# Kernel tuning notes

Measured on AMD Instinct MI355X. Metric: run time of the kernel, lower is better.

## Reference

```python
import jax, jax.numpy as jnp
import numpy as np

D_MODEL = 768
NUM_HEADS = 8
HEAD_DIM = D_MODEL // NUM_HEADS


def setup_inputs() -> dict:
    key = jax.random.key(0)
    ks = jax.random.split(key, 5)
    B, N = 4, 2048
    scale = 1.0 / np.sqrt(D_MODEL)
    return {
        "x": jax.random.normal(ks[0], (B, N, D_MODEL), dtype=jnp.float32),
        "W_qkv": jax.random.normal(ks[1], (D_MODEL, 3 * D_MODEL), dtype=jnp.float32) * scale,
        "b_qkv": jax.random.normal(ks[2], (3 * D_MODEL,), dtype=jnp.float32) * 0.01,
        "W_out": jax.random.normal(ks[3], (D_MODEL, D_MODEL), dtype=jnp.float32) * scale,
        "b_out": jax.random.normal(ks[4], (D_MODEL,), dtype=jnp.float32) * 0.01,
    }


def reference(x, W_qkv, b_qkv, W_out, b_out):
    B, N, _ = x.shape
    H, Dh = NUM_HEADS, HEAD_DIM
    # fused QKV projection: [B,N,3*D] -> [3,B,H,N,Dh]
    qkv = (x @ W_qkv + b_qkv).reshape(B, N, 3, H, Dh).transpose(2, 0, 3, 1, 4)
    q, k, v = qkv[0], qkv[1], qkv[2]
    # full NxN attention, as in the original (no masking)
    scores = jnp.einsum("bhnd,bhmd->bhnm", q, k) / jnp.sqrt(jnp.float32(Dh)).astype(x.dtype)
    weights = jax.nn.softmax(scores, axis=-1)
    out = jnp.einsum("bhnm,bhmd->bhnd", weights, v)  # [B,H,N,Dh]
    out = out.transpose(0, 2, 1, 3).reshape(B, N, H * Dh)
    return out @ W_out + b_out
```

## Files before the change

kernel.cpp:

```cpp
#include <hip/hip_runtime.h>
#include <hip/hip_bf16.h>
#include <math.h>

#define BB      4
#define NN      2048
#define DM      768
#define NH      8
#define DHH     96
#define BH      (BB*NH)
#define MROWS   (BB*NN)
#define NC_QKV  (3*DM)

typedef short v4s  __attribute__((ext_vector_type(4)));
typedef short v8s  __attribute__((ext_vector_type(8)));
typedef float v16f __attribute__((ext_vector_type(16)));
typedef unsigned int u32;

#define SCQ 0.14724599350930152f

static __device__ __forceinline__ ushort f2bf(float f) {
    __hip_bfloat16 h = __float2bfloat16(f);
    return *reinterpret_cast<ushort*>(&h);
}

static __device__ __forceinline__ void gload_lds16(const ushort* g, ushort* l) {
    __builtin_amdgcn_global_load_lds(
        (const __attribute__((address_space(1))) void*)g,
        (__attribute__((address_space(3))) void*)l, 16, 0, 0);
}

static __device__ __forceinline__ v8s load2x4(const ushort* p) {
    union { v4s h[2]; v8s s; } x;
    x.h[0] = *reinterpret_cast<const v4s*>(p);
    x.h[1] = *reinterpret_cast<const v4s*>(p + 8);
    return x.s;
}

static __device__ __forceinline__ v8s pack4(u32 a, u32 b, u32 c, u32 d) {
    union { u32 u[4]; v8s s; } x;
    x.u[0] = a; x.u[1] = b; x.u[2] = c; x.u[3] = d;
    return x.s;
}

__global__ __launch_bounds__(256)
void conv_bf16(const float* __restrict__ in, ushort* __restrict__ out, int n8)
{
    int i = blockIdx.x * 256 + threadIdx.x;
    if (i >= n8) return;
    const float4* p = reinterpret_cast<const float4*>(in) + (size_t)i * 2;
    float4 a = p[0], b = p[1];
    ushort r[8] = {f2bf(a.x), f2bf(a.y), f2bf(a.z), f2bf(a.w),
                   f2bf(b.x), f2bf(b.y), f2bf(b.z), f2bf(b.w)};
    *reinterpret_cast<v8s*>(out + (size_t)i * 8) = *reinterpret_cast<v8s*>(r);
}

__global__ __launch_bounds__(256)
void convT_bf16(const float* __restrict__ W, ushort* __restrict__ Wt, int K, int N)
{
    __shared__ ushort t[32][33];
    const int k0 = blockIdx.x * 32, n0 = blockIdx.y * 32;
    const int tx = threadIdx.x & 31, ty = threadIdx.x >> 5;
    #pragma unroll
    for (int r = ty; r < 32; r += 8)
        t[tx][r] = f2bf(W[(size_t)(k0 + r) * N + n0 + tx]);
    __syncthreads();
    #pragma unroll
    for (int r = ty; r < 32; r += 8)
        Wt[(size_t)(n0 + r) * K + k0 + tx] = t[r][tx];
}

template<int SCATTER>
__global__ __launch_bounds__(256)
void gemm_mfma(const ushort* __restrict__ A, const ushort* __restrict__ Bt,
               const float* __restrict__ bias, void* __restrict__ outp,
               int K, int Ncols)
{
    __shared__ ushort As[2][8192];
    __shared__ ushort Bs[2][8192];

    const int tid  = threadIdx.x;
    const int lane = tid & 63;
    const int wv   = tid >> 6;
    const int l31  = lane & 31;
    const int lhi  = lane >> 5;
    const int wr   = wv >> 1, wc = wv & 1;

    const int ny   = gridDim.y;
    const int id   = blockIdx.y * gridDim.x + blockIdx.x;
    const int c8   = id & 7;
    const int j    = id >> 3;
    const int hy   = (j >= (ny >> 1) * 8) ? 1 : 0;
    const int w    = j - hy * (ny >> 1) * 8;
    const int bx   = c8 * 8 + (w & 7);
    const int by   = hy * (ny >> 1) + (w >> 3);
    const int row0 = bx * 128;
    const int col0 = by * 128;

    v16f acc[2][2];
    #pragma unroll
    for (int mi = 0; mi < 2; ++mi)
        #pragma unroll
        for (int nj = 0; nj < 2; ++nj)
            #pragma unroll
            for (int i = 0; i < 16; ++i) acc[mi][nj][i] = 0.0f;

#define STAGE_G(bsel, kk) do {                                                  \
    _Pragma("unroll")                                                           \
    for (int c = 0; c < 4; ++c) {                                               \
        const int g   = c * 4 + wv;                                             \
        const int idx = g * 64 + lane;                                          \
        const int ss  = idx >> 7, rr = idx & 127;                               \
        gload_lds16(&A [(size_t)(row0 + rr) * K + (kk) + ss * 8],               \
                    &As[bsel][g * 512]);                                        \
        gload_lds16(&Bt[(size_t)(col0 + rr) * K + (kk) + ss * 8],               \
                    &Bs[bsel][g * 512]);                                        \
    }                                                                           \
} while (0)

    STAGE_G(0, 0);
    __syncthreads();

    const int nk = K >> 6;
    for (int t = 0; t < nk; ++t) {
        const int cur = t & 1;
        if (t + 1 < nk) STAGE_G(cur ^ 1, (t + 1) << 6);

        #pragma unroll
        for (int s16 = 0; s16 < 4; ++s16) {
            const int ks = s16 * 2 + lhi;
            v8s a0 = *reinterpret_cast<const v8s*>(&As[cur][(size_t)(ks * 128 + 64 * wr + l31) * 8]);
            v8s a1 = *reinterpret_cast<const v8s*>(&As[cur][(size_t)(ks * 128 + 64 * wr + 32 + l31) * 8]);
            v8s b0 = *reinterpret_cast<const v8s*>(&Bs[cur][(size_t)(ks * 128 + 64 * wc + l31) * 8]);
            v8s b1 = *reinterpret_cast<const v8s*>(&Bs[cur][(size_t)(ks * 128 + 64 * wc + 32 + l31) * 8]);
            acc[0][0] = __builtin_amdgcn_mfma_f32_32x32x16_bf16(a0, b0, acc[0][0], 0, 0, 0);
            acc[0][1] = __builtin_amdgcn_mfma_f32_32x32x16_bf16(a0, b1, acc[0][1], 0, 0, 0);
            acc[1][0] = __builtin_amdgcn_mfma_f32_32x32x16_bf16(a1, b0, acc[1][0], 0, 0, 0);
            acc[1][1] = __builtin_amdgcn_mfma_f32_32x32x16_bf16(a1, b1, acc[1][1], 0, 0, 0);
        }
        __syncthreads();
    }
#undef STAGE_G

    #pragma unroll
    for (int nj = 0; nj < 2; ++nj) {
        const int c = col0 + 64 * wc + 32 * nj + l31;
        const float bv = bias[c];
        #pragma unroll
        for (int mi = 0; mi < 2; ++mi) {
            #pragma unroll
            for (int r = 0; r < 16; ++r) {
                const int m = row0 + 64 * wr + 32 * mi + (r & 3) + 8 * (r >> 2) + 4 * lhi;
                float v = acc[mi][nj][r] + bv;
                if (SCATTER) {
                    const int s   = c / DM;
                    const int rem = c - s * DM;
                    const int h   = rem / DHH;
                    const int d   = rem - h * DHH;
                    const int b   = m >> 11;
                    const int n   = m & (NN - 1);
                    if (s == 0) v *= SCQ;
                    ((ushort*)outp)[((size_t)(s * BH + b * NH + h) * NN + n) * DHH + d] = f2bf(v);
                } else {
                    ((float*)outp)[(size_t)m * Ncols + c] = v;
                }
            }
        }
    }
}

__global__ __launch_bounds__(256)
void attn_mfma(const ushort* __restrict__ qkv, ushort* __restrict__ attnout)
{
    __shared__ ushort Ks[2][6144];
    __shared__ ushort Vt[2][96][72];

    const int tid  = threadIdx.x;
    const int lane = tid & 63;
    const int wv   = tid >> 6;
    const int l31  = lane & 31;
    const int lhi  = lane >> 5;

    const int id   = blockIdx.y * gridDim.x + blockIdx.x;
    const int c8   = id & 7;
    const int j    = id >> 3;
    const int bh   = c8 * 4 + (j >> 4);
    const int q0   = (j & 15) * 128;
    const int b    = bh >> 3, h = bh & 7;

    const ushort* Qg = qkv + (size_t)bh * NN * DHH;
    const ushort* Kg = qkv + ((size_t)BH + bh) * NN * DHH;
    const ushort* Vg = qkv + ((size_t)2 * BH + bh) * NN * DHH;

    const int qr = q0 + wv * 32 + l31;
    v8s qf[6];
    #pragma unroll
    for (int kt = 0; kt < 6; ++kt)
        qf[kt] = *reinterpret_cast<const v8s*>(&Qg[(size_t)qr * DHH + kt * 16 + lhi * 8]);

    v16f o[3];
    #pragma unroll
    for (int dt = 0; dt < 3; ++dt)
        #pragma unroll
        for (int i = 0; i < 16; ++i) o[dt][i] = 0.0f;
    float ds4[4] = {0.0f, 0.0f, 0.0f, 0.0f};

    {
        v8s kr[3], vr[3];
        #pragma unroll
        for (int i = 0; i < 3; ++i) {
            kr[i] = *reinterpret_cast<const v8s*>(&Kg[(size_t)lane * DHH + (wv * 3 + i) * 8]);
            vr[i] = *reinterpret_cast<const v8s*>(&Vg[(size_t)lane * DHH + (i * 4 + wv) * 8]);
        }
        #pragma unroll
        for (int i = 0; i < 3; ++i) {
            *reinterpret_cast<v8s*>(&Ks[0][(wv * 3 + i) * 512 + lane * 8]) = kr[i];
            #pragma unroll
            for (int j2 = 0; j2 < 8; ++j2)
                Vt[0][(i * 4 + wv) * 8 + j2][lane] = (ushort)vr[i][j2];
        }
    }
    __syncthreads();

    for (int t = 0; t < 32; ++t) {
        const int cur = t & 1, nxt = cur ^ 1;
        const int kbase = (t + 1) * 64;

        v8s kr0, kr1, kr2, vr0, vr1, vr2;
        if (t < 31) {
            const ushort* krow = &Kg[(size_t)(kbase + lane) * DHH];
            const ushort* vrow = &Vg[(size_t)(kbase + lane) * DHH];
            kr0 = *reinterpret_cast<const v8s*>(&krow[(wv * 3 + 0) * 8]);
            kr1 = *reinterpret_cast<const v8s*>(&krow[(wv * 3 + 1) * 8]);
            kr2 = *reinterpret_cast<const v8s*>(&krow[(wv * 3 + 2) * 8]);
            vr0 = *reinterpret_cast<const v8s*>(&vrow[(0 * 4 + wv) * 8]);
            vr1 = *reinterpret_cast<const v8s*>(&vrow[(1 * 4 + wv) * 8]);
            vr2 = *reinterpret_cast<const v8s*>(&vrow[(2 * 4 + wv) * 8]);
        }

        #pragma unroll
        for (int ct = 0; ct < 2; ++ct) {
            v16f s;
            #pragma unroll
            for (int i = 0; i < 16; ++i) s[i] = 0.0f;
            __builtin_amdgcn_s_setprio(1);
            #pragma unroll
            for (int kt = 0; kt < 6; ++kt) {
                v8s kf = *reinterpret_cast<const v8s*>(
                    &Ks[cur][((kt * 2 + lhi) * 64 + ct * 32 + l31) * 8]);
                s = __builtin_amdgcn_mfma_f32_32x32x16_bf16(kf, qf[kt], s, 0, 0, 0);
            }
            __builtin_amdgcn_s_setprio(0);

            float e[16];
            #pragma unroll
            for (int r = 0; r < 16; ++r) {
                e[r] = exp2f(s[r]);
                ds4[r & 3] += e[r];
            }
            u32 w[8];
            #pragma unroll
            for (int i = 0; i < 8; ++i)
                w[i] = (u32)f2bf(e[2 * i]) | ((u32)f2bf(e[2 * i + 1]) << 16);
            v8s pfA = pack4(w[0], w[1], w[2], w[3]);
            v8s pfB = pack4(w[4], w[5], w[6], w[7]);

            __builtin_amdgcn_s_setprio(1);
            #pragma unroll
            for (int dt = 0; dt < 3; ++dt) {
                const ushort* vp = &Vt[cur][dt * 32 + l31][ct * 32 + 4 * lhi];
                v8s vaA = load2x4(vp);
                v8s vaB = load2x4(vp + 16);
                o[dt] = __builtin_amdgcn_mfma_f32_32x32x16_bf16(vaA, pfA, o[dt], 0, 0, 0);
                o[dt] = __builtin_amdgcn_mfma_f32_32x32x16_bf16(vaB, pfB, o[dt], 0, 0, 0);
            }
            __builtin_amdgcn_s_setprio(0);
        }

        if (t < 31) {
            *reinterpret_cast<v8s*>(&Ks[nxt][(wv * 3 + 0) * 512 + lane * 8]) = kr0;
            *reinterpret_cast<v8s*>(&Ks[nxt][(wv * 3 + 1) * 512 + lane * 8]) = kr1;
            *reinterpret_cast<v8s*>(&Ks[nxt][(wv * 3 + 2) * 512 + lane * 8]) = kr2;
            #pragma unroll
            for (int j2 = 0; j2 < 8; ++j2) Vt[nxt][(0 * 4 + wv) * 8 + j2][lane] = (ushort)vr0[j2];
            #pragma unroll
            for (int j2 = 0; j2 < 8; ++j2) Vt[nxt][(1 * 4 + wv) * 8 + j2][lane] = (ushort)vr1[j2];
            #pragma unroll
            for (int j2 = 0; j2 < 8; ++j2) Vt[nxt][(2 * 4 + wv) * 8 + j2][lane] = (ushort)vr2[j2];
        }
        __syncthreads();
    }

    float dsum = (ds4[0] + ds4[1]) + (ds4[2] + ds4[3]);
    dsum += __shfl_xor(dsum, 32, 64);
    const float inv = 1.0f / dsum;

    const int n = q0 + wv * 32 + l31;
    ushort* orow = attnout + ((size_t)(b * NN + n)) * DM + h * DHH;
    #pragma unroll
    for (int dt = 0; dt < 3; ++dt) {
        #pragma unroll
        for (int g = 0; g < 4; ++g) {
            const int d0 = dt * 32 + 8 * g + 4 * lhi;
            u32 w0 = (u32)f2bf(o[dt][4 * g + 0] * inv) | ((u32)f2bf(o[dt][4 * g + 1] * inv) << 16);
            u32 w1 = (u32)f2bf(o[dt][4 * g + 2] * inv) | ((u32)f2bf(o[dt][4 * g + 3] * inv) << 16);
            uint2 pk; pk.x = w0; pk.y = w1;
            *reinterpret_cast<uint2*>(&orow[d0]) = pk;
        }
    }
}

extern "C" void kernel_launch(void* const* d_in, const int* in_sizes, int n_in,
                              void* d_out, int out_size, void* d_ws, size_t ws_size,
                              hipStream_t stream)
{
    (void)in_sizes; (void)n_in; (void)out_size; (void)ws_size;
    const float* x    = (const float*)d_in[0];
    const float* Wqkv = (const float*)d_in[1];
    const float* bqkv = (const float*)d_in[2];
    const float* Wout = (const float*)d_in[3];
    const float* bout = (const float*)d_in[4];
    float* out = (float*)d_out;

    ushort* qkv   = (ushort*)d_ws;
    ushort* ao    = qkv   + (size_t)3 * BH * NN * DHH;
    ushort* xbf   = ao    + (size_t)MROWS * DM;
    ushort* wqkvt = xbf   + (size_t)MROWS * DM;
    ushort* woutt = wqkvt + (size_t)DM * NC_QKV;

    dim3 blk(256);

    conv_bf16<<<dim3(MROWS * DM / 8 / 256), blk, 0, stream>>>(x, xbf, MROWS * DM / 8);
    convT_bf16<<<dim3(DM / 32, NC_QKV / 32), blk, 0, stream>>>(Wqkv, wqkvt, DM, NC_QKV);
    convT_bf16<<<dim3(DM / 32, DM / 32), blk, 0, stream>>>(Wout, woutt, DM, DM);

    gemm_mfma<1><<<dim3(MROWS / 128, NC_QKV / 128), blk, 0, stream>>>(
        xbf, wqkvt, bqkv, (void*)qkv, DM, NC_QKV);

    attn_mfma<<<dim3(NN / 128, BH), blk, 0, stream>>>(qkv, ao);

    gemm_mfma<0><<<dim3(MROWS / 128, DM / 128), blk, 0, stream>>>(
        ao, woutt, bout, (void*)out, DM, DM);
}
```

Before: 207.3 us.

## Split attention over key halves with 512-thread blocks and add combine kernel

The attention kernel now processes 256 query rows per 512-thread block and splits the key sequence into two halves across a grid z dimension. Each half writes unnormalized bf16 partial outputs and per-row exp sums, and a new combine kernel sums the partials and normalizes them. K and V loading is split between wave groups, and the double-buffered LDS becomes a single buffer guarded by two barriers. The intent is more parallel blocks and less LDS per block, at the cost of an extra pass over the output, extra bf16 rounding of the partials, and exposed load latency from the single buffer. Reusing the xbf workspace as a partial buffer relies on xbf being dead after the QKV GEMM.

```diff
diff --git a/kernel.cpp b/kernel.cpp
--- a/kernel.cpp
+++ b/kernel.cpp
@@ -21,6 +21,10 @@
 static __device__ __forceinline__ ushort f2bf(float f) {
     __hip_bfloat16 h = __float2bfloat16(f);
     return *reinterpret_cast<ushort*>(&h);
+}
+static __device__ __forceinline__ float bf2f(ushort u) {
+    u32 x = ((u32)u) << 16;
+    return __uint_as_float(x);
 }
 
 static __device__ __forceinline__ void gload_lds16(const ushort* g, ushort* l) {
@@ -168,23 +172,29 @@
     }
 }
 
-__global__ __launch_bounds__(256)
-void attn_mfma(const ushort* __restrict__ qkv, ushort* __restrict__ attnout)
-{
-    __shared__ ushort Ks[2][6144];
-    __shared__ ushort Vt[2][96][72];
+__global__ __launch_bounds__(512, 4)
+void attn_mfma(const ushort* __restrict__ qkv,
+               ushort* __restrict__ O0, ushort* __restrict__ O1,
+               float* __restrict__ dsw)
+{
+    __shared__ ushort Ks[6144];
+    __shared__ ushort Vt[96][68];
 
     const int tid  = threadIdx.x;
     const int lane = tid & 63;
     const int wv   = tid >> 6;
+    const int w2   = wv & 3;
     const int l31  = lane & 31;
     const int lhi  = lane >> 5;
 
-    const int id   = blockIdx.y * gridDim.x + blockIdx.x;
+    const int id   = blockIdx.z * (gridDim.x * gridDim.y)
+                   + blockIdx.y * gridDim.x + blockIdx.x;
     const int c8   = id & 7;
     const int j    = id >> 3;
-    const int bh   = c8 * 4 + (j >> 4);
-    const int q0   = (j & 15) * 128;
+    const int bh   = c8 * 4 + (j & 3);
+    const int qt   = (j >> 2) & 7;
+    const int half = j >> 5;
+    const int q0   = qt * 256;
     const int b    = bh >> 3, h = bh & 7;
 
     const ushort* Qg = qkv + (size_t)bh * NN * DHH;
@@ -204,37 +214,46 @@
         for (int i = 0; i < 16; ++i) o[dt][i] = 0.0f;
     float ds4[4] = {0.0f, 0.0f, 0.0f, 0.0f};
 
+    const int ts = half * 16, te = ts + 16;
+
     {
-        v8s kr[3], vr[3];
-        #pragma unroll
-        for (int i = 0; i < 3; ++i) {
-            kr[i] = *reinterpret_cast<const v8s*>(&Kg[(size_t)lane * DHH + (wv * 3 + i) * 8]);
-            vr[i] = *reinterpret_cast<const v8s*>(&Vg[(size_t)lane * DHH + (i * 4 + wv) * 8]);
-        }
-        #pragma unroll
-        for (int i = 0; i < 3; ++i) {
-            *reinterpret_cast<v8s*>(&Ks[0][(wv * 3 + i) * 512 + lane * 8]) = kr[i];
-            #pragma unroll
-            for (int j2 = 0; j2 < 8; ++j2)
-                Vt[0][(i * 4 + wv) * 8 + j2][lane] = (ushort)vr[i][j2];
+        const size_t rowb = (size_t)(ts * 64 + lane) * DHH;
+        if (wv < 4) {
+            v8s k0r = *reinterpret_cast<const v8s*>(&Kg[rowb + (w2 * 3 + 0) * 8]);
+            v8s k1r = *reinterpret_cast<const v8s*>(&Kg[rowb + (w2 * 3 + 1) * 8]);
+            v8s k2r = *reinterpret_cast<const v8s*>(&Kg[rowb + (w2 * 3 + 2) * 8]);
+            *reinterpret_cast<v8s*>(&Ks[(w2 * 3 + 0) * 512 + lane * 8]) = k0r;
+            *reinterpret_cast<v8s*>(&Ks[(w2 * 3 + 1) * 512 + lane * 8]) = k1r;
+            *reinterpret_cast<v8s*>(&Ks[(w2 * 3 + 2) * 512 + lane * 8]) = k2r;
+        } else {
+            v8s v0r = *reinterpret_cast<const v8s*>(&Vg[rowb + (0 * 4 + w2) * 8]);
+            v8s v1r = *reinterpret_cast<const v8s*>(&Vg[rowb + (1 * 4 + w2) * 8]);
+            v8s v2r = *reinterpret_cast<const v8s*>(&Vg[rowb + (2 * 4 + w2) * 8]);
+            #pragma unroll
+            for (int jj = 0; jj < 8; ++jj) Vt[(0 * 4 + w2) * 8 + jj][lane] = (ushort)v0r[jj];
+            #pragma unroll
+            for (int jj = 0; jj < 8; ++jj) Vt[(1 * 4 + w2) * 8 + jj][lane] = (ushort)v1r[jj];
+            #pragma unroll
+            for (int jj = 0; jj < 8; ++jj) Vt[(2 * 4 + w2) * 8 + jj][lane] = (ushort)v2r[jj];
         }
     }
     __syncthreads();
 
-    for (int t = 0; t < 32; ++t) {
-        const int cur = t & 1, nxt = cur ^ 1;
-        const int kbase = (t + 1) * 64;
-
-        v8s kr0, kr1, kr2, vr0, vr1, vr2;
-        if (t < 31) {
-            const ushort* krow = &Kg[(size_t)(kbase + lane) * DHH];
-            const ushort* vrow = &Vg[(size_t)(kbase + lane) * DHH];
-            kr0 = *reinterpret_cast<const v8s*>(&krow[(wv * 3 + 0) * 8]);
-            kr1 = *reinterpret_cast<const v8s*>(&krow[(wv * 3 + 1) * 8]);
-            kr2 = *reinterpret_cast<const v8s*>(&krow[(wv * 3 + 2) * 8]);
-            vr0 = *reinterpret_cast<const v8s*>(&vrow[(0 * 4 + wv) * 8]);
-            vr1 = *reinterpret_cast<const v8s*>(&vrow[(1 * 4 + wv) * 8]);
-            vr2 = *reinterpret_cast<const v8s*>(&vrow[(2 * 4 + wv) * 8]);
+    for (int t = ts; t < te; ++t) {
+        const bool have = (t + 1 < te);
+
+        v8s r0, r1, r2;
+        if (have) {
+            const size_t rowb = (size_t)((t + 1) * 64 + lane) * DHH;
+            if (wv < 4) {
+                r0 = *reinterpret_cast<const v8s*>(&Kg[rowb + (w2 * 3 + 0) * 8]);
+                r1 = *reinterpret_cast<const v8s*>(&Kg[rowb + (w2 * 3 + 1) * 8]);
+                r2 = *reinterpret_cast<const v8s*>(&Kg[rowb + (w2 * 3 + 2) * 8]);
+            } else {
+                r0 = *reinterpret_cast<const v8s*>(&Vg[rowb + (0 * 4 + w2) * 8]);
+                r1 = *reinterpret_cast<const v8s*>(&Vg[rowb + (1 * 4 + w2) * 8]);
+                r2 = *reinterpret_cast<const v8s*>(&Vg[rowb + (2 * 4 + w2) * 8]);
+            }
         }
 
         #pragma unroll
@@ -246,7 +265,7 @@
             #pragma unroll
             for (int kt = 0; kt < 6; ++kt) {
                 v8s kf = *reinterpret_cast<const v8s*>(
-                    &Ks[cur][((kt * 2 + lhi) * 64 + ct * 32 + l31) * 8]);
+                    &Ks[((kt * 2 + lhi) * 64 + ct * 32 + l31) * 8]);
                 s = __builtin_amdgcn_mfma_f32_32x32x16_bf16(kf, qf[kt], s, 0, 0, 0);
             }
             __builtin_amdgcn_s_setprio(0);
@@ -267,7 +286,7 @@
             __builtin_amdgcn_s_setprio(1);
             #pragma unroll
             for (int dt = 0; dt < 3; ++dt) {
-                const ushort* vp = &Vt[cur][dt * 32 + l31][ct * 32 + 4 * lhi];
+                const ushort* vp = &Vt[dt * 32 + l31][ct * 32 + 4 * lhi];
                 v8s vaA = load2x4(vp);
                 v8s vaB = load2x4(vp + 16);
                 o[dt] = __builtin_amdgcn_mfma_f32_32x32x16_bf16(vaA, pfA, o[dt], 0, 0, 0);
@@ -276,37 +295,65 @@
             __builtin_amdgcn_s_setprio(0);
         }
 
-        if (t < 31) {
-            *reinterpret_cast<v8s*>(&Ks[nxt][(wv * 3 + 0) * 512 + lane * 8]) = kr0;
-            *reinterpret_cast<v8s*>(&Ks[nxt][(wv * 3 + 1) * 512 + lane * 8]) = kr1;
-            *reinterpret_cast<v8s*>(&Ks[nxt][(wv * 3 + 2) * 512 + lane * 8]) = kr2;
-            #pragma unroll
-            for (int j2 = 0; j2 < 8; ++j2) Vt[nxt][(0 * 4 + wv) * 8 + j2][lane] = (ushort)vr0[j2];
-            #pragma unroll
-            for (int j2 = 0; j2 < 8; ++j2) Vt[nxt][(1 * 4 + wv) * 8 + j2][lane] = (ushort)vr1[j2];
-            #pragma unroll
-            for (int j2 = 0; j2 < 8; ++j2) Vt[nxt][(2 * 4 + wv) * 8 + j2][lane] = (ushort)vr2[j2];
-        }
-        __syncthreads();
+        if (have) {
+            __syncthreads();
+            if (wv < 4) {
+                *reinterpret_cast<v8s*>(&Ks[(w2 * 3 + 0) * 512 + lane * 8]) = r0;
+                *reinterpret_cast<v8s*>(&Ks[(w2 * 3 + 1) * 512 + lane * 8]) = r1;
+                *reinterpret_cast<v8s*>(&Ks[(w2 * 3 + 2) * 512 + lane * 8]) = r2;
+            } else {
+                #pragma unroll
+                for (int jj = 0; jj < 8; ++jj) Vt[(0 * 4 + w2) * 8 + jj][lane] = (ushort)r0[jj];
+                #pragma unroll
+                for (int jj = 0; jj < 8; ++jj) Vt[(1 * 4 + w2) * 8 + jj][lane] = (ushort)r1[jj];
+                #pragma unroll
+                for (int jj = 0; jj < 8; ++jj) Vt[(2 * 4 + w2) * 8 + jj][lane] = (ushort)r2[jj];
+            }
+            __syncthreads();
+        }
     }
 
     float dsum = (ds4[0] + ds4[1]) + (ds4[2] + ds4[3]);
     dsum += __shfl_xor(dsum, 32, 64);
-    const float inv = 1.0f / dsum;
+    if (lane < 32)
+        dsw[(size_t)half * BH * NN + (size_t)bh * NN + q0 + wv * 32 + lane] = dsum;
 
     const int n = q0 + wv * 32 + l31;
-    ushort* orow = attnout + ((size_t)(b * NN + n)) * DM + h * DHH;
+    ushort* orow = (half ? O1 : O0) + ((size_t)(b * NN + n)) * DM + h * DHH;
     #pragma unroll
     for (int dt = 0; dt < 3; ++dt) {
         #pragma unroll
         for (int g = 0; g < 4; ++g) {
             const int d0 = dt * 32 + 8 * g + 4 * lhi;
-            u32 w0 = (u32)f2bf(o[dt][4 * g + 0] * inv) | ((u32)f2bf(o[dt][4 * g + 1] * inv) << 16);
-            u32 w1 = (u32)f2bf(o[dt][4 * g + 2] * inv) | ((u32)f2bf(o[dt][4 * g + 3] * inv) << 16);
+            u32 w0 = (u32)f2bf(o[dt][4 * g + 0]) | ((u32)f2bf(o[dt][4 * g + 1]) << 16);
+            u32 w1 = (u32)f2bf(o[dt][4 * g + 2]) | ((u32)f2bf(o[dt][4 * g + 3]) << 16);
             uint2 pk; pk.x = w0; pk.y = w1;
             *reinterpret_cast<uint2*>(&orow[d0]) = pk;
         }
     }
+}
+
+__global__ __launch_bounds__(256)
+void combine_kernel(const ushort* __restrict__ O0, ushort* __restrict__ O1io,
+                    const float* __restrict__ dsw)
+{
+    const int i = blockIdx.x * 256 + threadIdx.x;
+    const int row = i / 96;
+    const int c   = i - row * 96;
+    const int h   = c / 12;
+    const int b   = row >> 11;
+    const int n   = row & (NN - 1);
+    const int bh  = b * NH + h;
+    const float d0 = dsw[(size_t)bh * NN + n];
+    const float d1 = dsw[(size_t)BH * NN + (size_t)bh * NN + n];
+    const float inv = 1.0f / (d0 + d1);
+    v8s a  = *reinterpret_cast<const v8s*>(&O0[(size_t)i * 8]);
+    v8s bb = *reinterpret_cast<v8s*>(&O1io[(size_t)i * 8]);
+    ushort r[8];
+    #pragma unroll
+    for (int jj = 0; jj < 8; ++jj)
+        r[jj] = f2bf((bf2f((ushort)a[jj]) + bf2f((ushort)bb[jj])) * inv);
+    *reinterpret_cast<v8s*>(&O1io[(size_t)i * 8]) = *reinterpret_cast<v8s*>(r);
 }
 
 extern "C" void kernel_launch(void* const* d_in, const int* in_sizes, int n_in,
@@ -326,6 +373,7 @@
     ushort* xbf   = ao    + (size_t)MROWS * DM;
     ushort* wqkvt = xbf   + (size_t)MROWS * DM;
     ushort* woutt = wqkvt + (size_t)DM * NC_QKV;
+    float*  dsw   = (float*)(woutt + (size_t)DM * DM);
 
     dim3 blk(256);
 
@@ -336,7 +384,9 @@
     gemm_mfma<1><<<dim3(MROWS / 128, NC_QKV / 128), blk, 0, stream>>>(
         xbf, wqkvt, bqkv, (void*)qkv, DM, NC_QKV);
 
-    attn_mfma<<<dim3(NN / 128, BH), blk, 0, stream>>>(qkv, ao);
+    attn_mfma<<<dim3(8, 32, 2), dim3(512), 0, stream>>>(qkv, xbf, ao, dsw);
+
+    combine_kernel<<<dim3(MROWS * DM / 8 / 256), blk, 0, stream>>>(xbf, ao, dsw);
 
     gemm_mfma<0><<<dim3(MROWS / 128, DM / 128), blk, 0, stream>>>(
         ao, woutt, bout, (void*)out, DM, DM);
```

After: 261.1 us. +26.0%, slower.

## Switch attention to 16x16x32 MFMA with 64-row query tiles and single-buffered LDS

Applied to the files above, without the earlier changes.

Rewrites the attention kernel to use 16x16x32 bf16 MFMAs with 16 query rows per wave (64 per block), doubling the grid to 1024 blocks. The LDS K/V buffers go from double-buffered to single-buffered, and launch bounds request 4 blocks per CU. The aim is more occupancy and fewer registers per wave so latency hides better. In exchange, each K/V tile is loaded by twice as many blocks, and the loop now has two barriers per iteration instead of one.

```diff
diff --git a/kernel.cpp b/kernel.cpp
--- a/kernel.cpp
+++ b/kernel.cpp
@@ -13,6 +13,7 @@
 
 typedef short v4s  __attribute__((ext_vector_type(4)));
 typedef short v8s  __attribute__((ext_vector_type(8)));
+typedef float v4f  __attribute__((ext_vector_type(4)));
 typedef float v16f __attribute__((ext_vector_type(16)));
 typedef unsigned int u32;
 
@@ -29,10 +30,10 @@
         (__attribute__((address_space(3))) void*)l, 16, 0, 0);
 }
 
-static __device__ __forceinline__ v8s load2x4(const ushort* p) {
+static __device__ __forceinline__ v8s load2x4_o16(const ushort* p) {
     union { v4s h[2]; v8s s; } x;
     x.h[0] = *reinterpret_cast<const v4s*>(p);
-    x.h[1] = *reinterpret_cast<const v4s*>(p + 8);
+    x.h[1] = *reinterpret_cast<const v4s*>(p + 16);
     return x.s;
 }
 
@@ -40,6 +41,9 @@
     union { u32 u[4]; v8s s; } x;
     x.u[0] = a; x.u[1] = b; x.u[2] = c; x.u[3] = d;
     return x.s;
+}
+static __device__ __forceinline__ u32 bfpair(float lo, float hi) {
+    return (u32)f2bf(lo) | ((u32)f2bf(hi) << 16);
 }
 
 __global__ __launch_bounds__(256)
@@ -168,144 +172,138 @@
     }
 }
 
-__global__ __launch_bounds__(256)
+__global__ __launch_bounds__(256, 4)
 void attn_mfma(const ushort* __restrict__ qkv, ushort* __restrict__ attnout)
 {
-    __shared__ ushort Ks[2][6144];
-    __shared__ ushort Vt[2][96][72];
+    __shared__ ushort Ks[6144];
+    __shared__ ushort Vt[96][68];
 
     const int tid  = threadIdx.x;
     const int lane = tid & 63;
     const int wv   = tid >> 6;
-    const int l31  = lane & 31;
-    const int lhi  = lane >> 5;
+    const int l15  = lane & 15;
+    const int g4   = lane >> 4;
 
     const int id   = blockIdx.y * gridDim.x + blockIdx.x;
     const int c8   = id & 7;
     const int j    = id >> 3;
-    const int bh   = c8 * 4 + (j >> 4);
-    const int q0   = (j & 15) * 128;
+    const int bh   = c8 * 4 + (j & 3);
+    const int qt   = j >> 2;
+    const int q0   = qt * 64;
     const int b    = bh >> 3, h = bh & 7;
 
     const ushort* Qg = qkv + (size_t)bh * NN * DHH;
     const ushort* Kg = qkv + ((size_t)BH + bh) * NN * DHH;
     const ushort* Vg = qkv + ((size_t)2 * BH + bh) * NN * DHH;
 
-    const int qr = q0 + wv * 32 + l31;
-    v8s qf[6];
-    #pragma unroll
-    for (int kt = 0; kt < 6; ++kt)
-        qf[kt] = *reinterpret_cast<const v8s*>(&Qg[(size_t)qr * DHH + kt * 16 + lhi * 8]);
-
-    v16f o[3];
-    #pragma unroll
-    for (int dt = 0; dt < 3; ++dt)
-        #pragma unroll
-        for (int i = 0; i < 16; ++i) o[dt][i] = 0.0f;
-    float ds4[4] = {0.0f, 0.0f, 0.0f, 0.0f};
+    const int qrow = q0 + wv * 16 + l15;
+    v8s qf[3];
+    #pragma unroll
+    for (int c = 0; c < 3; ++c)
+        qf[c] = *reinterpret_cast<const v8s*>(&Qg[(size_t)qrow * DHH + c * 32 + g4 * 8]);
+
+    v4f o[6];
+    #pragma unroll
+    for (int dt = 0; dt < 6; ++dt)
+        #pragma unroll
+        for (int i = 0; i < 4; ++i) o[dt][i] = 0.0f;
+    float ds = 0.0f;
 
     {
+        const size_t rowb = (size_t)lane * DHH;
         v8s kr[3], vr[3];
         #pragma unroll
         for (int i = 0; i < 3; ++i) {
-            kr[i] = *reinterpret_cast<const v8s*>(&Kg[(size_t)lane * DHH + (wv * 3 + i) * 8]);
-            vr[i] = *reinterpret_cast<const v8s*>(&Vg[(size_t)lane * DHH + (i * 4 + wv) * 8]);
+            kr[i] = *reinterpret_cast<const v8s*>(&Kg[rowb + (wv * 3 + i) * 8]);
+            vr[i] = *reinterpret_cast<const v8s*>(&Vg[rowb + (i * 4 + wv) * 8]);
         }
         #pragma unroll
         for (int i = 0; i < 3; ++i) {
-            *reinterpret_cast<v8s*>(&Ks[0][(wv * 3 + i) * 512 + lane * 8]) = kr[i];
-            #pragma unroll
-            for (int j2 = 0; j2 < 8; ++j2)
-                Vt[0][(i * 4 + wv) * 8 + j2][lane] = (ushort)vr[i][j2];
+            *reinterpret_cast<v8s*>(&Ks[(wv * 3 + i) * 512 + lane * 8]) = kr[i];
+            #pragma unroll
+            for (int jj = 0; jj < 8; ++jj)
+                Vt[(i * 4 + wv) * 8 + jj][lane] = (ushort)vr[i][jj];
         }
     }
     __syncthreads();
 
     for (int t = 0; t < 32; ++t) {
-        const int cur = t & 1, nxt = cur ^ 1;
-        const int kbase = (t + 1) * 64;
-
         v8s kr0, kr1, kr2, vr0, vr1, vr2;
         if (t < 31) {
-            const ushort* krow = &Kg[(size_t)(kbase + lane) * DHH];
-            const ushort* vrow = &Vg[(size_t)(kbase + lane) * DHH];
-            kr0 = *reinterpret_cast<const v8s*>(&krow[(wv * 3 + 0) * 8]);
-            kr1 = *reinterpret_cast<const v8s*>(&krow[(wv * 3 + 1) * 8]);
-            kr2 = *reinterpret_cast<const v8s*>(&krow[(wv * 3 + 2) * 8]);
-            vr0 = *reinterpret_cast<const v8s*>(&vrow[(0 * 4 + wv) * 8]);
-            vr1 = *reinterpret_cast<const v8s*>(&vrow[(1 * 4 + wv) * 8]);
-            vr2 = *reinterpret_cast<const v8s*>(&vrow[(2 * 4 + wv) * 8]);
-        }
-
-        #pragma unroll
-        for (int ct = 0; ct < 2; ++ct) {
-            v16f s;
-            #pragma unroll
-            for (int i = 0; i < 16; ++i) s[i] = 0.0f;
+            const size_t rowb = (size_t)((t + 1) * 64 + lane) * DHH;
+            kr0 = *reinterpret_cast<const v8s*>(&Kg[rowb + (wv * 3 + 0) * 8]);
+            kr1 = *reinterpret_cast<const v8s*>(&Kg[rowb + (wv * 3 + 1) * 8]);
+            kr2 = *reinterpret_cast<const v8s*>(&Kg[rowb + (wv * 3 + 2) * 8]);
+            vr0 = *reinterpret_cast<const v8s*>(&Vg[rowb + (0 * 4 + wv) * 8]);
+            vr1 = *reinterpret_cast<const v8s*>(&Vg[rowb + (1 * 4 + wv) * 8]);
+            vr2 = *reinterpret_cast<const v8s*>(&Vg[rowb + (2 * 4 + wv) * 8]);
+        }
+
+        #pragma unroll
+        for (int th = 0; th < 2; ++th) {
+            v4f s0, s1;
+            #pragma unroll
+            for (int i = 0; i < 4; ++i) { s0[i] = 0.0f; s1[i] = 0.0f; }
             __builtin_amdgcn_s_setprio(1);
             #pragma unroll
-            for (int kt = 0; kt < 6; ++kt) {
-                v8s kf = *reinterpret_cast<const v8s*>(
-                    &Ks[cur][((kt * 2 + lhi) * 64 + ct * 32 + l31) * 8]);
-                s = __builtin_amdgcn_mfma_f32_32x32x16_bf16(kf, qf[kt], s, 0, 0, 0);
+            for (int c = 0; c < 3; ++c) {
+                v8s kf0 = *reinterpret_cast<const v8s*>(
+                    &Ks[((c * 4 + g4) * 64 + (th * 2 + 0) * 16 + l15) * 8]);
+                v8s kf1 = *reinterpret_cast<const v8s*>(
+                    &Ks[((c * 4 + g4) * 64 + (th * 2 + 1) * 16 + l15) * 8]);
+                s0 = __builtin_amdgcn_mfma_f32_16x16x32_bf16(kf0, qf[c], s0, 0, 0, 0);
+                s1 = __builtin_amdgcn_mfma_f32_16x16x32_bf16(kf1, qf[c], s1, 0, 0, 0);
             }
             __builtin_amdgcn_s_setprio(0);
 
-            float e[16];
-            #pragma unroll
-            for (int r = 0; r < 16; ++r) {
-                e[r] = exp2f(s[r]);
-                ds4[r & 3] += e[r];
+            float e0[4], e1[4];
+            #pragma unroll
+            for (int r = 0; r < 4; ++r) {
+                e0[r] = exp2f(s0[r]);
+                e1[r] = exp2f(s1[r]);
+                ds += e0[r] + e1[r];
             }
-            u32 w[8];
-            #pragma unroll
-            for (int i = 0; i < 8; ++i)
-                w[i] = (u32)f2bf(e[2 * i]) | ((u32)f2bf(e[2 * i + 1]) << 16);
-            v8s pfA = pack4(w[0], w[1], w[2], w[3]);
-            v8s pfB = pack4(w[4], w[5], w[6], w[7]);
+            v8s pf = pack4(bfpair(e0[0], e0[1]), bfpair(e0[2], e0[3]),
+                           bfpair(e1[0], e1[1]), bfpair(e1[2], e1[3]));
 
             __builtin_amdgcn_s_setprio(1);
             #pragma unroll
-            for (int dt = 0; dt < 3; ++dt) {
-                const ushort* vp = &Vt[cur][dt * 32 + l31][ct * 32 + 4 * lhi];
-                v8s vaA = load2x4(vp);
-                v8s vaB = load2x4(vp + 16);
-                o[dt] = __builtin_amdgcn_mfma_f32_32x32x16_bf16(vaA, pfA, o[dt], 0, 0, 0);
-                o[dt] = __builtin_amdgcn_mfma_f32_32x32x16_bf16(vaB, pfB, o[dt], 0, 0, 0);
+            for (int dt = 0; dt < 6; ++dt) {
+                const ushort* vp = &Vt[dt * 16 + l15][th * 32 + g4 * 4];
+                v8s va = load2x4_o16(vp);
+                o[dt] = __builtin_amdgcn_mfma_f32_16x16x32_bf16(va, pf, o[dt], 0, 0, 0);
             }
             __builtin_amdgcn_s_setprio(0);
         }
 
         if (t < 31) {
-            *reinterpret_cast<v8s*>(&Ks[nxt][(wv * 3 + 0) * 512 + lane * 8]) = kr0;
-            *reinterpret_cast<v8s*>(&Ks[nxt][(wv * 3 + 1) * 512 + lane * 8]) = kr1;
-            *reinterpret_cast<v8s*>(&Ks[nxt][(wv * 3 + 2) * 512 + lane * 8]) = kr2;
-            #pragma unroll
-            for (int j2 = 0; j2 < 8; ++j2) Vt[nxt][(0 * 4 + wv) * 8 + j2][lane] = (ushort)vr0[j2];
-            #pragma unroll
-            for (int j2 = 0; j2 < 8; ++j2) Vt[nxt][(1 * 4 + wv) * 8 + j2][lane] = (ushort)vr1[j2];
-            #pragma unroll
-            for (int j2 = 0; j2 < 8; ++j2) Vt[nxt][(2 * 4 + wv) * 8 + j2][lane] = (ushort)vr2[j2];
-        }
-        __syncthreads();
-    }
-
-    float dsum = (ds4[0] + ds4[1]) + (ds4[2] + ds4[3]);
-    dsum += __shfl_xor(dsum, 32, 64);
-    const float inv = 1.0f / dsum;
-
-    const int n = q0 + wv * 32 + l31;
+            __syncthreads();
+            *reinterpret_cast<v8s*>(&Ks[(wv * 3 + 0) * 512 + lane * 8]) = kr0;
+            *reinterpret_cast<v8s*>(&Ks[(wv * 3 + 1) * 512 + lane * 8]) = kr1;
+            *reinterpret_cast<v8s*>(&Ks[(wv * 3 + 2) * 512 + lane * 8]) = kr2;
+            #pragma unroll
+            for (int jj = 0; jj < 8; ++jj) Vt[(0 * 4 + wv) * 8 + jj][lane] = (ushort)vr0[jj];
+            #pragma unroll
+            for (int jj = 0; jj < 8; ++jj) Vt[(1 * 4 + wv) * 8 + jj][lane] = (ushort)vr1[jj];
+            #pragma unroll
+            for (int jj = 0; jj < 8; ++jj) Vt[(2 * 4 + wv) * 8 + jj][lane] = (ushort)vr2[jj];
+            __syncthreads();
+        }
+    }
+
+    ds += __shfl_xor(ds, 16, 64);
+    ds += __shfl_xor(ds, 32, 64);
+    const float inv = 1.0f / ds;
+
+    const int n = q0 + wv * 16 + l15;
     ushort* orow = attnout + ((size_t)(b * NN + n)) * DM + h * DHH;
     #pragma unroll
-    for (int dt = 0; dt < 3; ++dt) {
-        #pragma unroll
-        for (int g = 0; g < 4; ++g) {
-            const int d0 = dt * 32 + 8 * g + 4 * lhi;
-            u32 w0 = (u32)f2bf(o[dt][4 * g + 0] * inv) | ((u32)f2bf(o[dt][4 * g + 1] * inv) << 16);
-            u32 w1 = (u32)f2bf(o[dt][4 * g + 2] * inv) | ((u32)f2bf(o[dt][4 * g + 3] * inv) << 16);
-            uint2 pk; pk.x = w0; pk.y = w1;
-            *reinterpret_cast<uint2*>(&orow[d0]) = pk;
-        }
+    for (int dt = 0; dt < 6; ++dt) {
+        const int d0 = dt * 16 + g4 * 4;
+        uint2 pk;
+        pk.x = bfpair(o[dt][0] * inv, o[dt][1] * inv);
+        pk.y = bfpair(o[dt][2] * inv, o[dt][3] * inv);
+        *reinterpret_cast<uint2*>(&orow[d0]) = pk;
     }
 }
 
@@ -336,7 +334,7 @@
     gemm_mfma<1><<<dim3(MROWS / 128, NC_QKV / 128), blk, 0, stream>>>(
         xbf, wqkvt, bqkv, (void*)qkv, DM, NC_QKV);
 
-    attn_mfma<<<dim3(NN / 128, BH), blk, 0, stream>>>(qkv, ao);
+    attn_mfma<<<dim3(32, 32), blk, 0, stream>>>(qkv, ao);
 
     gemm_mfma<0><<<dim3(MROWS / 128, DM / 128), blk, 0, stream>>>(
         ao, woutt, bout, (void*)out, DM, DM);
```

New measurement: 209.2 us. No clear change (+0.9%).
